# Optimization experiments

Hardware: AMD Instinct MI355X
Metric: run time of the kernel (lower is better)

Reference implementation:

```python
import jax, jax.numpy as jnp
import numpy as np

B, S, W, H = 16, 512, 8, 768  # batch, seq_len, max_span width, hidden_dim


def setup_inputs() -> dict:
    key = jax.random.key(0)
    ks = jax.random.split(key, 6)
    return {
        "hidden": jax.random.normal(ks[0], (B, S, H), jnp.float32),
        "term_weight": jax.random.normal(ks[1], (H,), jnp.float32),
        "w1": jax.random.normal(ks[2], (H, 64), jnp.float32) * 0.02,
        "b1": jnp.zeros((64,), jnp.float32),
        "w2": jax.random.normal(ks[3], (64, 1), jnp.float32) * 0.05,
        "b2": jnp.zeros((1,), jnp.float32),
        "w_score": jax.random.normal(ks[4], (H, 2), jnp.float32) * 0.02,
        "b_score": jnp.zeros((2,), jnp.float32),
    }


def reference(hidden, term_weight, w1, b1, w2, b2, w_score, b_score):
    # TermAttention token logits: MLP(hidden * termWeight) depends only on the
    # token, not the span, so compute once per token instead of per span.
    ah = hidden * term_weight                                  # [B,S,H]
    tok_logit = (jax.nn.relu(ah @ w1 + b1) @ w2 + b2)[..., 0]  # [B,S]

    starts = jnp.arange(S)
    offs = jnp.arange(W)
    # candidate span (start s, width w) covers tokens s .. min(s+w, S-1)
    tok_idx = jnp.minimum(starts[:, None] + offs[None, :], S - 1)      # [S,W]
    span_len = jnp.minimum(offs[None, :] + 1, S - starts[:, None])    # [S,W]

    Lg = tok_logit[:, tok_idx]   # [B,S,W] gathered per-position logits
    Hg = hidden[:, tok_idx]      # [B,S,W,H] gathered per-position hiddens

    # pos_mask[s,w,j] = position j is inside span (s, width w)
    pos_mask = offs[None, None, :] < span_len[:, :, None]              # [S,W,W]
    logits = jnp.where(pos_mask[None], Lg[:, :, None, :], -jnp.inf)   # [B,S,W,W]
    attn = jax.nn.softmax(logits, axis=-1)                             # [B,S,W,W]

    # span embedding = attention-weighted sum of span token hiddens
    emb = jnp.einsum('bswj,bsjh->bswh', attn, Hg)                      # [B,S,W,H]
    scores = emb @ w_score + b_score                                   # [B,S,W,2]
    return scores
```

## Files before the change

kernel.cpp:

```cpp
#include <hip/hip_runtime.h>
#include <hip/hip_bf16.h>

#define S_LEN 512
#define H_DIM 768
#define BS_TOK 8192
#define NCOLS 80
#define KSPLIT 4
#define KSEG 192
#define PSTRIDE 72
#define TOKB 32
#define FRAG_ELEMS (KSPLIT * 6 * 5 * 64 * 8)

typedef __attribute__((ext_vector_type(8))) short short8v;
typedef __attribute__((ext_vector_type(4))) short short4v;
typedef __attribute__((ext_vector_type(4))) float f32x4;
typedef __attribute__((ext_vector_type(4))) _Float16 h4;

__device__ __forceinline__ short f2bf(float f) {
  union { float f; unsigned u; } x; x.f = f;
  unsigned r = x.u + 0x7fffu + ((x.u >> 16) & 1u);
  return (short)(r >> 16);
}

__device__ __forceinline__ short bfc(float f) {
  __hip_bfloat16 b = __float2bfloat16(f);
  return *reinterpret_cast<short*>(&b);
}

__global__ __launch_bounds__(256) void kprepF(const float* __restrict__ tw,
                                              const float* __restrict__ w1,
                                              const float* __restrict__ wsc,
                                              short* __restrict__ wf) {
  int i = blockIdx.x * 256 + threadIdx.x;
  if (i >= FRAG_ELEMS) return;
  int e    = i & 7;
  int lane = (i >> 3) & 63;
  int rest = i >> 9;
  int nt   = rest % 5;
  int sk   = rest / 5;
  int k    = sk * 32 + (lane >> 4) * 8 + e;
  int c    = nt * 16 + (lane & 15);
  float v = 0.f;
  if (c < 64)       v = tw[k] * w1[(size_t)k * 64 + c];
  else if (c < 66)  v = wsc[(size_t)k * 2 + (c - 64)];
  wf[i] = f2bf(v);
}

__global__ __launch_bounds__(256) void kG(const float* __restrict__ hidden,
                                          const short* __restrict__ wf,
                                          _Float16* __restrict__ part) {
  const int tid  = threadIdx.x;
  const int wv   = blockIdx.x * 4 + (tid >> 6);
  const int lane = tid & 63;
  const int seg  = wv & 3;
  const int tile = wv >> 2;
  const int ci   = lane & 15;
  const int g    = lane >> 4;
  const int r0   = tile * 16;

  const float* aptr = hidden + (size_t)(r0 + ci) * H_DIM + seg * KSEG + g * 8;
  float4 abuf[12];
#pragma unroll
  for (int q = 0; q < 6; ++q) {
    abuf[2 * q]     = *reinterpret_cast<const float4*>(aptr + q * 32);
    abuf[2 * q + 1] = *reinterpret_cast<const float4*>(aptr + q * 32 + 4);
  }

  const short8v* bf = reinterpret_cast<const short8v*>(wf) + (size_t)seg * 6 * 5 * 64 + lane;

  f32x4 acc[5];
#pragma unroll
  for (int nt = 0; nt < 5; ++nt) acc[nt] = (f32x4){0.f, 0.f, 0.f, 0.f};

#pragma unroll
  for (int ks = 0; ks < 6; ++ks) {
    const float4 a0 = abuf[2 * ks];
    const float4 a1 = abuf[2 * ks + 1];
    short8v av;
    av[0] = bfc(a0.x); av[1] = bfc(a0.y); av[2] = bfc(a0.z); av[3] = bfc(a0.w);
    av[4] = bfc(a1.x); av[5] = bfc(a1.y); av[6] = bfc(a1.z); av[7] = bfc(a1.w);
#pragma unroll
    for (int nt = 0; nt < 5; ++nt) {
      short8v bb = bf[(ks * 5 + nt) * 64];
      acc[nt] = __builtin_amdgcn_mfma_f32_16x16x32_bf16(av, bb, acc[nt], 0, 0, 0);
    }
  }

  _Float16* pr = part + ((size_t)seg * BS_TOK + r0) * PSTRIDE;
#pragma unroll
  for (int j = 0; j < 4; ++j) {
    int r = 4 * g + j;
#pragma unroll
    for (int nt = 0; nt < 4; ++nt)
      pr[r * PSTRIDE + nt * 16 + ci] = (_Float16)acc[nt][j];
    if (ci < 2) pr[r * PSTRIDE + 64 + ci] = (_Float16)acc[4][j];
  }
}

__global__ __launch_bounds__(256) void kB(const _Float16* __restrict__ part,
                                          const float* __restrict__ b1,
                                          const float* __restrict__ w2,
                                          const float* __restrict__ b2,
                                          const float* __restrict__ bsc,
                                          float* __restrict__ out) {
  __shared__ float lp[TOKB + 8][4];
  const int tid  = threadIdx.x;
  const int t0   = blockIdx.x * TOKB;
  const int w    = tid >> 6;
  const int lane = tid & 63;
  const int ci   = lane & 15;
  const int grp  = lane >> 4;
  const int base = w * 4 + grp;

#pragma unroll
  for (int pass = 0; pass < 3; ++pass) {
    int slot = pass * 16 + base;
    if (slot < TOKB + 7) {
      int tt = min(t0 + slot, BS_TOK - 1);
      h4 v[KSPLIT];
#pragma unroll
      for (int seg = 0; seg < KSPLIT; ++seg)
        v[seg] = *reinterpret_cast<const h4*>(
            part + ((size_t)seg * BS_TOK + tt) * PSTRIDE + 4 * ci);
      f32x4 s = (f32x4){0.f, 0.f, 0.f, 0.f};
#pragma unroll
      for (int seg = 0; seg < KSPLIT; ++seg) {
        s[0] += (float)v[seg][0]; s[1] += (float)v[seg][1];
        s[2] += (float)v[seg][2]; s[3] += (float)v[seg][3];
      }
      float pv = 0.f;
      if (ci < 2) {
#pragma unroll
        for (int seg = 0; seg < KSPLIT; ++seg)
          pv += (float)part[((size_t)seg * BS_TOK + tt) * PSTRIDE + 64 + ci];
      }
      const float4 bb = *reinterpret_cast<const float4*>(b1 + 4 * ci);
      const float4 ww = *reinterpret_cast<const float4*>(w2 + 4 * ci);
      float r = fmaxf(s[0] + bb.x, 0.f) * ww.x + fmaxf(s[1] + bb.y, 0.f) * ww.y +
                fmaxf(s[2] + bb.z, 0.f) * ww.z + fmaxf(s[3] + bb.w, 0.f) * ww.w;
#pragma unroll
      for (int msk = 1; msk < 16; msk <<= 1) r += __shfl_xor(r, msk, 64);
      if (ci == 0) lp[slot][0] = r + b2[0];
      if (ci < 2)  lp[slot][1 + ci] = pv;
    }
  }
  __syncthreads();

  if (tid < TOKB) {
    int t = t0 + tid;
    int s_ = t & (S_LEN - 1);
    int nmax = min(8, S_LEN - s_);
    float bs0 = bsc[0], bs1 = bsc[1];
    float m = lp[tid][0];
    float d = 1.f;
    float n0 = lp[tid][1], n1 = lp[tid][2];
    float o[16];
    o[0] = n0 + bs0; o[1] = n1 + bs1;
#pragma unroll
    for (int j = 1; j < 8; ++j) {
      if (j < nmax) {
        float L  = lp[tid + j][0];
        float nm = fmaxf(m, L);
        float sc = __expf(m - nm);
        float e  = __expf(L - nm);
        d  = d  * sc + e;
        n0 = n0 * sc + e * lp[tid + j][1];
        n1 = n1 * sc + e * lp[tid + j][2];
        m = nm;
      }
      float inv = 1.f / d;
      o[2 * j]     = n0 * inv + bs0;
      o[2 * j + 1] = n1 * inv + bs1;
    }
    float4* op = reinterpret_cast<float4*>(out + (size_t)t * 16);
#pragma unroll
    for (int i = 0; i < 4; ++i) op[i] = *reinterpret_cast<float4*>(&o[4 * i]);
  }
}


__global__ __launch_bounds__(256) void kprepS(const float* __restrict__ tw,
                                              const float* __restrict__ w1,
                                              const float* __restrict__ wsc,
                                              short* __restrict__ wcat) {
  int i = blockIdx.x * 256 + threadIdx.x;
  if (i >= NCOLS * H_DIM) return;
  int c = i / H_DIM, k = i - c * H_DIM;
  float v = 0.f;
  if (c < 64)       v = tw[k] * w1[k * 64 + c];
  else if (c == 64) v = wsc[k * 2 + 0];
  else if (c == 65) v = wsc[k * 2 + 1];
  wcat[i] = f2bf(v);
}

__global__ __launch_bounds__(256) void k1s(const float* __restrict__ hidden,
                                           const short* __restrict__ wcat,
                                           const float* __restrict__ b1,
                                           const float* __restrict__ w2,
                                           const float* __restrict__ b2,
                                           float* __restrict__ logit,
                                           float* __restrict__ pbuf) {
  __shared__ short as[64 * 72];
  __shared__ short bss[NCOLS * 72];
  const int tid  = threadIdx.x;
  const int t0   = blockIdx.x * 64;
  const int w    = tid >> 6;
  const int lane = tid & 63;
  const int ci   = lane & 15;
  const int kg   = (lane >> 4) * 8;
  const int arow = w * 16 + ci;

  f32x4 acc[5];
#pragma unroll
  for (int nt = 0; nt < 5; ++nt) acc[nt] = (f32x4){0.f, 0.f, 0.f, 0.f};

  for (int cc = 0; cc < H_DIM / 64; ++cc) {
    const int k0 = cc * 64;
    __syncthreads();
#pragma unroll
    for (int i = 0; i < 4; ++i) {
      int f = tid + 256 * i;
      int r = f >> 4, c4 = f & 15;
      const float4 v = *reinterpret_cast<const float4*>(
          hidden + (size_t)(t0 + r) * H_DIM + k0 + c4 * 4);
      short4v bv;
      bv[0] = f2bf(v.x); bv[1] = f2bf(v.y); bv[2] = f2bf(v.z); bv[3] = f2bf(v.w);
      *reinterpret_cast<short4v*>(&as[r * 72 + c4 * 4]) = bv;
    }
    for (int i = tid; i < NCOLS * 8; i += 256) {
      int r = i >> 3, c8 = i & 7;
      short8v v = *reinterpret_cast<const short8v*>(wcat + r * H_DIM + k0 + c8 * 8);
      *reinterpret_cast<short8v*>(&bss[r * 72 + c8 * 8]) = v;
    }
    __syncthreads();
#pragma unroll
    for (int ks = 0; ks < 64; ks += 32) {
      short8v a = *reinterpret_cast<const short8v*>(&as[arow * 72 + ks + kg]);
#pragma unroll
      for (int nt = 0; nt < 5; ++nt) {
        short8v bb = *reinterpret_cast<const short8v*>(&bss[(nt * 16 + ci) * 72 + ks + kg]);
        acc[nt] = __builtin_amdgcn_mfma_f32_16x16x32_bf16(a, bb, acc[nt], 0, 0, 0);
      }
    }
  }

  const int g = lane >> 4;
  float lg[4];
#pragma unroll
  for (int j = 0; j < 4; ++j) {
    float sacc = 0.f;
#pragma unroll
    for (int nt = 0; nt < 4; ++nt) {
      int c = nt * 16 + ci;
      float z = acc[nt][j] + b1[c];
      z = fmaxf(z, 0.f);
      sacc += z * w2[c];
    }
#pragma unroll
    for (int msk = 1; msk < 16; msk <<= 1) sacc += __shfl_xor(sacc, msk, 64);
    lg[j] = sacc;
  }
  const float b2v = b2[0];
#pragma unroll
  for (int j = 0; j < 4; ++j) {
    int rg = t0 + w * 16 + 4 * g + j;
    if (ci == 0) {
      logit[rg] = lg[j] + b2v;
      pbuf[rg * 2 + 0] = acc[4][j];
    } else if (ci == 1) {
      pbuf[rg * 2 + 1] = acc[4][j];
    }
  }
}

__global__ __launch_bounds__(256) void k3g(const float* __restrict__ logit,
                                           const float* __restrict__ pbuf,
                                           const float* __restrict__ bsc,
                                           float* __restrict__ out) {
  int t = blockIdx.x * 256 + threadIdx.x;
  int s = t & (S_LEN - 1);
  int nmax = min(8, S_LEN - s);
  float bs0 = bsc[0], bs1 = bsc[1];
  float m = logit[t];
  float d = 1.f;
  float n0 = pbuf[2 * t], n1 = pbuf[2 * t + 1];
  float o[16];
  o[0] = n0 + bs0; o[1] = n1 + bs1;
#pragma unroll
  for (int j = 1; j < 8; ++j) {
    if (j < nmax) {
      float L  = logit[t + j];
      float nm = fmaxf(m, L);
      float sc = __expf(m - nm);
      float e  = __expf(L - nm);
      d  = d  * sc + e;
      n0 = n0 * sc + e * pbuf[2 * (t + j)];
      n1 = n1 * sc + e * pbuf[2 * (t + j) + 1];
      m = nm;
    }
    float inv = 1.f / d;
    o[2 * j]     = n0 * inv + bs0;
    o[2 * j + 1] = n1 * inv + bs1;
  }
  float4* op = reinterpret_cast<float4*>(out + (size_t)t * 16);
#pragma unroll
  for (int i = 0; i < 4; ++i) op[i] = *reinterpret_cast<float4*>(&o[4 * i]);
}


extern "C" void kernel_launch(void* const* d_in, const int* in_sizes, int n_in,
                              void* d_out, int out_size, void* d_ws, size_t ws_size,
                              hipStream_t stream) {
  const float* hidden = (const float*)d_in[0];
  const float* tw     = (const float*)d_in[1];
  const float* w1     = (const float*)d_in[2];
  const float* b1     = (const float*)d_in[3];
  const float* w2     = (const float*)d_in[4];
  const float* b2     = (const float*)d_in[5];
  const float* wsc    = (const float*)d_in[6];
  const float* bsc    = (const float*)d_in[7];
  float* out = (float*)d_out;
  char* ws = (char*)d_ws;

  const size_t part_bytes = (size_t)KSPLIT * BS_TOK * PSTRIDE * 2;
  const size_t frag_bytes = (size_t)FRAG_ELEMS * 2;
  const size_t need_fast  = part_bytes + frag_bytes;

  if (ws_size >= need_fast) {
    _Float16* part = (_Float16*)ws;
    short* wf      = (short*)(ws + part_bytes);
    kprepF<<<(FRAG_ELEMS + 255) / 256, 256, 0, stream>>>(tw, w1, wsc, wf);
    kG    <<<BS_TOK * KSPLIT / 16 / 4, 256, 0, stream>>>(hidden, wf, part);
    kB    <<<BS_TOK / TOKB, 256, 0, stream>>>(part, b1, w2, b2, bsc, out);
  } else {
    short* wcat  = (short*)ws;
    float* logit = (float*)(ws + 131072);
    float* pbuf  = (float*)(ws + 131072 + 32768);
    kprepS<<<(NCOLS * H_DIM + 255) / 256, 256, 0, stream>>>(tw, w1, wsc, wcat);
    k1s<<<BS_TOK / 64, 256, 0, stream>>>(hidden, wcat, b1, w2, b2, logit, pbuf);
    k3g<<<BS_TOK / 256, 256, 0, stream>>>(logit, pbuf, bsc, out);
  }
}
```

Before: 22.95 us.

## Fuse MFMA projection and span epilogue into one kernel with LDS K-split reduction

Merges the bf16 MFMA projection kernel and the span softmax/scoring kernel into a single 384-thread kernel. Each block computes 48 token rows (its 32 tokens plus a halo for the span window) with two K-halves per row tile, and reduces the halves through shared memory instead of writing fp16 partials to global workspace. This removes one launch and the global round trip of the partial sums. In exchange, each wave keeps twice as many hidden values in registers, and halo rows are recomputed redundantly across neighbouring blocks.

```diff
diff --git a/kernel.cpp b/kernel.cpp
--- a/kernel.cpp
+++ b/kernel.cpp
@@ -5,16 +5,14 @@
 #define H_DIM 768
 #define BS_TOK 8192
 #define NCOLS 80
-#define KSPLIT 4
-#define KSEG 192
-#define PSTRIDE 72
 #define TOKB 32
-#define FRAG_ELEMS (KSPLIT * 6 * 5 * 64 * 8)
+#define ROWS 48
+#define RPAD 81
+#define FRAG_ELEMS (4 * 6 * 5 * 64 * 8)
 
 typedef __attribute__((ext_vector_type(8))) short short8v;
 typedef __attribute__((ext_vector_type(4))) short short4v;
 typedef __attribute__((ext_vector_type(4))) float f32x4;
-typedef __attribute__((ext_vector_type(4))) _Float16 h4;
 
 __device__ __forceinline__ short f2bf(float f) {
   union { float f; unsigned u; } x; x.f = f;
@@ -46,34 +44,42 @@
   wf[i] = f2bf(v);
 }
 
-__global__ __launch_bounds__(256) void kG(const float* __restrict__ hidden,
+__global__ __launch_bounds__(384) void kF(const float* __restrict__ hidden,
                                           const short* __restrict__ wf,
-                                          _Float16* __restrict__ part) {
+                                          const float* __restrict__ b1,
+                                          const float* __restrict__ w2,
+                                          const float* __restrict__ b2,
+                                          const float* __restrict__ bsc,
+                                          float* __restrict__ out) {
+  __shared__ float red[ROWS][RPAD];
+  __shared__ float lp[ROWS][4];
+
   const int tid  = threadIdx.x;
-  const int wv   = blockIdx.x * 4 + (tid >> 6);
+  const int t0   = blockIdx.x * TOKB;
+  const int w    = tid >> 6;
   const int lane = tid & 63;
-  const int seg  = wv & 3;
-  const int tile = wv >> 2;
   const int ci   = lane & 15;
   const int g    = lane >> 4;
-  const int r0   = tile * 16;
-
-  const float* aptr = hidden + (size_t)(r0 + ci) * H_DIM + seg * KSEG + g * 8;
-  float4 abuf[12];
-#pragma unroll
-  for (int q = 0; q < 6; ++q) {
+  const int tile = w % 3;
+  const int h    = w / 3;
+  const int rrow = min(t0 + tile * 16 + ci, BS_TOK - 1);
+
+  const float* aptr = hidden + (size_t)rrow * H_DIM + h * 384 + g * 8;
+  float4 abuf[24];
+#pragma unroll
+  for (int q = 0; q < 12; ++q) {
     abuf[2 * q]     = *reinterpret_cast<const float4*>(aptr + q * 32);
     abuf[2 * q + 1] = *reinterpret_cast<const float4*>(aptr + q * 32 + 4);
   }
 
-  const short8v* bf = reinterpret_cast<const short8v*>(wf) + (size_t)seg * 6 * 5 * 64 + lane;
+  const short8v* bfv = reinterpret_cast<const short8v*>(wf) + (size_t)h * 12 * 5 * 64 + lane;
 
   f32x4 acc[5];
 #pragma unroll
   for (int nt = 0; nt < 5; ++nt) acc[nt] = (f32x4){0.f, 0.f, 0.f, 0.f};
 
 #pragma unroll
-  for (int ks = 0; ks < 6; ++ks) {
+  for (int ks = 0; ks < 12; ++ks) {
     const float4 a0 = abuf[2 * ks];
     const float4 a1 = abuf[2 * ks + 1];
     short8v av;
@@ -81,67 +87,45 @@
     av[4] = bfc(a1.x); av[5] = bfc(a1.y); av[6] = bfc(a1.z); av[7] = bfc(a1.w);
 #pragma unroll
     for (int nt = 0; nt < 5; ++nt) {
-      short8v bb = bf[(ks * 5 + nt) * 64];
+      short8v bb = bfv[(ks * 5 + nt) * 64];
       acc[nt] = __builtin_amdgcn_mfma_f32_16x16x32_bf16(av, bb, acc[nt], 0, 0, 0);
     }
   }
 
-  _Float16* pr = part + ((size_t)seg * BS_TOK + r0) * PSTRIDE;
-#pragma unroll
-  for (int j = 0; j < 4; ++j) {
-    int r = 4 * g + j;
-#pragma unroll
-    for (int nt = 0; nt < 4; ++nt)
-      pr[r * PSTRIDE + nt * 16 + ci] = (_Float16)acc[nt][j];
-    if (ci < 2) pr[r * PSTRIDE + 64 + ci] = (_Float16)acc[4][j];
-  }
-}
-
-__global__ __launch_bounds__(256) void kB(const _Float16* __restrict__ part,
-                                          const float* __restrict__ b1,
-                                          const float* __restrict__ w2,
-                                          const float* __restrict__ b2,
-                                          const float* __restrict__ bsc,
-                                          float* __restrict__ out) {
-  __shared__ float lp[TOKB + 8][4];
-  const int tid  = threadIdx.x;
-  const int t0   = blockIdx.x * TOKB;
-  const int w    = tid >> 6;
-  const int lane = tid & 63;
-  const int ci   = lane & 15;
-  const int grp  = lane >> 4;
-  const int base = w * 4 + grp;
-
-#pragma unroll
-  for (int pass = 0; pass < 3; ++pass) {
-    int slot = pass * 16 + base;
-    if (slot < TOKB + 7) {
-      int tt = min(t0 + slot, BS_TOK - 1);
-      h4 v[KSPLIT];
-#pragma unroll
-      for (int seg = 0; seg < KSPLIT; ++seg)
-        v[seg] = *reinterpret_cast<const h4*>(
-            part + ((size_t)seg * BS_TOK + tt) * PSTRIDE + 4 * ci);
-      f32x4 s = (f32x4){0.f, 0.f, 0.f, 0.f};
-#pragma unroll
-      for (int seg = 0; seg < KSPLIT; ++seg) {
-        s[0] += (float)v[seg][0]; s[1] += (float)v[seg][1];
-        s[2] += (float)v[seg][2]; s[3] += (float)v[seg][3];
+  if (h == 1) {
+#pragma unroll
+    for (int j = 0; j < 4; ++j) {
+      int r = tile * 16 + 4 * g + j;
+#pragma unroll
+      for (int nt = 0; nt < 5; ++nt)
+        red[r][nt * 16 + ci] = acc[nt][j];
+    }
+  }
+  __syncthreads();
+
+  if (h == 0) {
+    float b1c[4], w2c[4];
+#pragma unroll
+    for (int nt = 0; nt < 4; ++nt) {
+      b1c[nt] = b1[nt * 16 + ci];
+      w2c[nt] = w2[nt * 16 + ci];
+    }
+    const float b2v = b2[0];
+#pragma unroll
+    for (int j = 0; j < 4; ++j) {
+      int r = tile * 16 + 4 * g + j;
+      float s = 0.f;
+#pragma unroll
+      for (int nt = 0; nt < 4; ++nt) {
+        float z = acc[nt][j] + red[r][nt * 16 + ci] + b1c[nt];
+        z = fmaxf(z, 0.f);
+        s += z * w2c[nt];
       }
-      float pv = 0.f;
-      if (ci < 2) {
-#pragma unroll
-        for (int seg = 0; seg < KSPLIT; ++seg)
-          pv += (float)part[((size_t)seg * BS_TOK + tt) * PSTRIDE + 64 + ci];
-      }
-      const float4 bb = *reinterpret_cast<const float4*>(b1 + 4 * ci);
-      const float4 ww = *reinterpret_cast<const float4*>(w2 + 4 * ci);
-      float r = fmaxf(s[0] + bb.x, 0.f) * ww.x + fmaxf(s[1] + bb.y, 0.f) * ww.y +
-                fmaxf(s[2] + bb.z, 0.f) * ww.z + fmaxf(s[3] + bb.w, 0.f) * ww.w;
-#pragma unroll
-      for (int msk = 1; msk < 16; msk <<= 1) r += __shfl_xor(r, msk, 64);
-      if (ci == 0) lp[slot][0] = r + b2[0];
-      if (ci < 2)  lp[slot][1 + ci] = pv;
+#pragma unroll
+      for (int msk = 1; msk < 16; msk <<= 1) s += __shfl_xor(s, msk, 64);
+      float pv = acc[4][j] + red[r][64 + ci];
+      if (ci == 0) lp[r][0] = s + b2v;
+      if (ci < 2)  lp[r][1 + ci] = pv;
     }
   }
   __syncthreads();
@@ -322,16 +306,12 @@
   float* out = (float*)d_out;
   char* ws = (char*)d_ws;
 
-  const size_t part_bytes = (size_t)KSPLIT * BS_TOK * PSTRIDE * 2;
   const size_t frag_bytes = (size_t)FRAG_ELEMS * 2;
-  const size_t need_fast  = part_bytes + frag_bytes;
-
-  if (ws_size >= need_fast) {
-    _Float16* part = (_Float16*)ws;
-    short* wf      = (short*)(ws + part_bytes);
+
+  if (ws_size >= frag_bytes) {
+    short* wf = (short*)ws;
     kprepF<<<(FRAG_ELEMS + 255) / 256, 256, 0, stream>>>(tw, w1, wsc, wf);
-    kG    <<<BS_TOK * KSPLIT / 16 / 4, 256, 0, stream>>>(hidden, wf, part);
-    kB    <<<BS_TOK / TOKB, 256, 0, stream>>>(part, b1, w2, b2, bsc, out);
+    kF    <<<BS_TOK / TOKB, 384, 0, stream>>>(hidden, wf, b1, w2, b2, bsc, out);
   } else {
     short* wcat  = (short*)ws;
     float* logit = (float*)(ws + 131072);
```

Result: no change. 23.37 us (+1.8%).
